# Kernel tuning notes

Measured on AMD Instinct MI355X. Metric: run time of the kernel, lower is better.

## Reference

```python
import jax, jax.numpy as jnp
import numpy as np

NUM_CELLS = 91
NUM_MOVES = 4206
D = 64
NH = 4
HD = D // NH  # 16
FF = 2 * D   # 128
FILTERS = 128

# static hex grid indices (same as torch _hex_grid_indices)
_idx = [(r + 5, q + 5) for q in range(-5, 6) for r in range(-5, 6)
        if max(abs(q), abs(r), abs(q + r)) <= 5]
_HEX_ROWS = np.array([r for r, c in _idx], dtype=np.int32)
_HEX_COLS = np.array([c for r, c in _idx], dtype=np.int32)


def _ln(x, g, b, eps=1e-5):
    m = jnp.mean(x, axis=-1, keepdims=True)
    v = jnp.mean((x - m) ** 2, axis=-1, keepdims=True)
    return (x - m) * jax.lax.rsqrt(v + eps) * g + b


def setup_inputs() -> dict:
    key = jax.random.key(0)
    ks = jax.random.split(key, 24)
    B = 512
    s = lambda fan_in: 1.0 / np.sqrt(fan_in)
    return {
        "x": jax.random.normal(ks[0], (B, FILTERS, 11, 11), dtype=jnp.float32),
        "embed_w": jax.random.uniform(ks[1], (D, FILTERS), minval=-s(FILTERS), maxval=s(FILTERS)),
        "embed_b": jax.random.uniform(ks[2], (D,), minval=-s(FILTERS), maxval=s(FILTERS)),
        "pos": jax.random.normal(ks[3], (1, NUM_CELLS, D)) * 0.02,
        "in_w": jax.random.uniform(ks[4], (3 * D, D), minval=-s(D), maxval=s(D)),
        "in_b": jnp.zeros((3 * D,), jnp.float32),
        "out_w": jax.random.uniform(ks[5], (D, D), minval=-s(D), maxval=s(D)),
        "out_b": jnp.zeros((D,), jnp.float32),
        "ln1_g": jnp.ones((D,), jnp.float32),
        "ln1_b": jnp.zeros((D,), jnp.float32),
        "ln2_g": jnp.ones((D,), jnp.float32),
        "ln2_b": jnp.zeros((D,), jnp.float32),
        "ff1_w": jax.random.uniform(ks[6], (FF, D), minval=-s(D), maxval=s(D)),
        "ff1_b": jax.random.uniform(ks[7], (FF,), minval=-s(D), maxval=s(D)),
        "ff2_w": jax.random.uniform(ks[8], (D, FF), minval=-s(FF), maxval=s(FF)),
        "ff2_b": jax.random.uniform(ks[9], (D,), minval=-s(FF), maxval=s(FF)),
        "from_w": jax.random.uniform(ks[10], (D, D), minval=-s(D), maxval=s(D)),
        "from_b": jax.random.uniform(ks[11], (D,), minval=-s(D), maxval=s(D)),
        "to_w": jax.random.uniform(ks[12], (D, D), minval=-s(D), maxval=s(D)),
        "to_b": jax.random.uniform(ks[13], (D,), minval=-s(D), maxval=s(D)),
        "move_bias": jnp.zeros((NUM_MOVES,), jnp.float32),
        "move_from": jax.random.randint(ks[14], (NUM_MOVES,), 0, NUM_CELLS, dtype=jnp.int32),
        "move_to": jax.random.randint(ks[15], (NUM_MOVES,), 0, NUM_CELLS, dtype=jnp.int32),
    }


def reference(x, embed_w, embed_b, pos, in_w, in_b, out_w, out_b,
              ln1_g, ln1_b, ln2_g, ln2_b, ff1_w, ff1_b, ff2_w, ff2_b,
              from_w, from_b, to_w, to_b, move_bias, move_from, move_to):
    B = x.shape[0]
    # extract_hex: (B, C, 11, 11) -> (B, 91, C)
    feats = x[:, :, _HEX_ROWS, _HEX_COLS].transpose(0, 2, 1)
    h = feats @ embed_w.T + embed_b + pos  # (B, 91, D)

    # TransformerEncoderLayer, norm_first=True, eval (dropout=0), relu FFN
    hn = _ln(h, ln1_g, ln1_b)
    qkv = hn @ in_w.T + in_b  # (B, 91, 3D)
    q, k, v = jnp.split(qkv, 3, axis=-1)
    q = q.reshape(B, NUM_CELLS, NH, HD).transpose(0, 2, 1, 3)
    k = k.reshape(B, NUM_CELLS, NH, HD).transpose(0, 2, 1, 3)
    v = v.reshape(B, NUM_CELLS, NH, HD).transpose(0, 2, 1, 3)
    scores = jnp.einsum("bhqd,bhkd->bhqk", q, k) / np.sqrt(HD)
    attn = jax.nn.softmax(scores, axis=-1)
    o = jnp.einsum("bhqk,bhkd->bhqd", attn, v)
    o = o.transpose(0, 2, 1, 3).reshape(B, NUM_CELLS, D)
    h = h + (o @ out_w.T + out_b)
    hn = _ln(h, ln2_g, ln2_b)
    h = h + (jax.nn.relu(hn @ ff1_w.T + ff1_b) @ ff2_w.T + ff2_b)

    from_feats = h @ from_w.T + from_b  # (B, 91, D)
    to_feats = h @ to_w.T + to_b
    f = jnp.take(from_feats, move_from, axis=1)  # (B, 4206, D)
    t = jnp.take(to_feats, move_to, axis=1)      # (B, 4206, D)
    logits = jnp.sum(f * t, axis=-1) + move_bias  # (B, 4206)
    return logits
```

## Files before the change

### kernel.cpp

```cpp
#include <hip/hip_runtime.h>
#include <hip/hip_bf16.h>

typedef __attribute__((ext_vector_type(8))) short short8;
typedef __attribute__((ext_vector_type(4))) float f32x4;

#define NC    91
#define DM    64
#define CIN   128
#define NMOV  4206
#define MR    96
#define HP    68
#define NT    1024
#define NW    16
#define VTP   104

#define W_EMBED 0
#define W_IN    8192
#define W_OUT   20480
#define W_FF1   24576
#define W_FF2   32768
#define W_FT    40960
#define W_TOTAL 49152

__constant__ int HEXOFF[NC] = {
  55,66,77,88,99,110,
  45,56,67,78,89,100,111,
  35,46,57,68,79,90,101,112,
  25,36,47,58,69,80,91,102,113,
  15,26,37,48,59,70,81,92,103,114,
  5,16,27,38,49,60,71,82,93,104,115,
  6,17,28,39,50,61,72,83,94,105,
  7,18,29,40,51,62,73,84,95,
  8,19,30,41,52,63,74,85,
  9,20,31,42,53,64,75,
  10,21,32,43,54,65
};

#define SWZ(row, col, PB) ((row)*(PB) + ((((((col)*2)>>4)) ^ ((row)&7)) << 4) + (((col)*2)&15))

__device__ __forceinline__ short f2bf(float f) {
  __hip_bfloat16 h = __float2bfloat16(f);
  return __builtin_bit_cast(short, h);
}

__device__ __forceinline__ short8 ldfrag128(const short* buf, int row, int k0) {
  return *(const short8*)((const char*)buf + SWZ(row, k0, 128));
}
__device__ __forceinline__ short8 ldfrag256(const short* buf, int row, int k0) {
  return *(const short8*)((const char*)buf + SWZ(row, k0, 256));
}
__device__ __forceinline__ void stb16_128(short* buf, int row, int col, float v) {
  *(short*)((char*)buf + SWZ(row, col, 128)) = f2bf(v);
}
__device__ __forceinline__ void cp8_swz(short* dst, int PB, const short* src, int r, int c8, int K) {
  short8 v = *(const short8*)(src + r*K + c8*8);
  *(short8*)((char*)dst + r*PB + ((c8 ^ (r&7)) << 4)) = v;
}

__device__ __forceinline__ void ln_group(const float* hbuf, short* ab16,
                                         const float* gw, const float* gb,
                                         int wid, int lane) {
  const int sub = lane >> 4;
  const int l16 = lane & 15;
  const float4 g4 = *(const float4*)&gw[l16*4];
  const float4 b4 = *(const float4*)&gb[l16*4];
  for (int g = wid; g < 23; g += NW) {
    int i = g*4 + sub;
    if (i < NC) {
      float4 v = *(const float4*)&hbuf[i*HP + l16*4];
      float s  = (v.x + v.y) + (v.z + v.w);
      float sq = fmaf(v.x,v.x, fmaf(v.y,v.y, fmaf(v.z,v.z, v.w*v.w)));
      #pragma unroll
      for (int off = 1; off < 16; off <<= 1) {
        s  += __shfl_xor(s, off, 64);
        sq += __shfl_xor(sq, off, 64);
      }
      float m  = s * (1.0f/64.0f);
      float vr = sq * (1.0f/64.0f) - m*m;
      float rs = rsqrtf(vr + 1e-5f);
      short4 o;
      o.x = f2bf((v.x - m)*rs*g4.x + b4.x);
      o.y = f2bf((v.y - m)*rs*g4.y + b4.y);
      o.z = f2bf((v.z - m)*rs*g4.z + b4.z);
      o.w = f2bf((v.w - m)*rs*g4.w + b4.w);
      *(short4*)((char*)ab16 + i*128 + (((l16>>1) ^ (i&7))<<4) + (l16&1)*8) = o;
    }
  }
}

__global__ __launch_bounds__(256)
void prep_w(const float* __restrict__ embed_w, const float* __restrict__ in_w,
            const float* __restrict__ out_w, const float* __restrict__ ff1_w,
            const float* __restrict__ ff2_w, const float* __restrict__ from_w,
            const float* __restrict__ to_w, short* __restrict__ ws)
{
  int i = blockIdx.x*256 + threadIdx.x;
  if (i >= W_TOTAL) return;
  float v;
  if      (i < 8192)  v = embed_w[i];
  else if (i < 20480) v = in_w[i - 8192];
  else if (i < 24576) v = out_w[i - 20480];
  else if (i < 32768) v = ff1_w[i - 24576];
  else if (i < 40960) v = ff2_w[i - 32768];
  else if (i < 45056) v = from_w[i - 40960];
  else                v = to_w[i - 45056];
  ws[i] = f2bf(v);
}

__global__ __launch_bounds__(1024, 1)
void policy_fused(
    const float* __restrict__ x,
    const float* __restrict__ embed_b, const float* __restrict__ pos,
    const float* __restrict__ in_b,  const float* __restrict__ out_b,
    const float* __restrict__ ln1_g, const float* __restrict__ ln1_b,
    const float* __restrict__ ln2_g, const float* __restrict__ ln2_b,
    const float* __restrict__ ff1_b, const float* __restrict__ ff2_b,
    const float* __restrict__ from_b, const float* __restrict__ to_b,
    const float* __restrict__ move_bias,
    const int* __restrict__ move_from, const int* __restrict__ move_to,
    const short* __restrict__ ws,
    float* __restrict__ out)
{
  __shared__ float arena[18816];
  __shared__ float hbuf[MR*HP];
  __shared__ short ab16[MR*64];
  __shared__ short wAll[20480];
  __shared__ float lsum[384];

  const int tid  = threadIdx.x;
  const int lane = tid & 63;
  const int wid  = tid >> 6;
  const int l15  = lane & 15;
  const int kfr  = (lane >> 4) * 8;
  const int mfr  = (lane >> 4) * 4;
  const int b    = blockIdx.x;
  const float* xb = x + (size_t)b * (CIN*121);

  short* arena_s = (short*)arena;
  short* featsb = arena_s;
  short* qf     = arena_s + 24576;
  short* kf     = arena_s + 30720;
  short* vtb    = wAll;
  short* owst   = arena_s + 24576;
  short* f1     = arena_s + 18432;
  float* G      = arena;

  #define PALL_ROW(i) ((char*)((i) < 64 ? (void*)((char*)arena + (i)*768) \
                                        : (void*)((char*)wAll + 16384 + ((i)-64)*768)))

  for (int e = tid; e < 16*NC; e += NT) {
    int c0 = e / NC, i = e - c0*NC;
    float v[8];
    #pragma unroll
    for (int u = 0; u < 8; ++u) v[u] = xb[(c0*8 + u)*121 + HEXOFF[i]];
    short8 s8;
    #pragma unroll
    for (int u = 0; u < 8; ++u) s8[u] = f2bf(v[u]);
    *(short8*)((char*)featsb + i*256 + ((c0 ^ (i&7)) << 4)) = s8;
  }
  if (tid < 320) ((unsigned*)featsb)[5824 + tid] = 0;
  if (tid < 384) lsum[tid] = 0.f;
  for (int e = tid; e < 1024; e += NT) {
    int r = e >> 4, c8 = e & 15;
    cp8_swz(wAll, 256, ws + W_EMBED, r, c8, 128);
  }
  for (int e = tid; e < 1536; e += NT) {
    int r = e >> 3, c8 = e & 7;
    cp8_swz(wAll + 8192, 128, ws + W_IN, r, c8, 64);
  }
  __syncthreads();

  for (int t = wid; t < 24; t += NW) {
    int mt = t >> 2, nt = t & 3;
    int ar = mt*16 + l15, br = nt*16 + l15;
    f32x4 acc = {0.f,0.f,0.f,0.f};
    #pragma unroll
    for (int kk = 0; kk < 4; ++kk) {
      short8 a = ldfrag256(featsb, ar, kk*32 + kfr);
      short8 w = ldfrag256(wAll,   br, kk*32 + kfr);
      acc = __builtin_amdgcn_mfma_f32_16x16x32_bf16(a, w, acc, 0, 0, 0);
    }
    int col = nt*16 + l15;
    float eb = embed_b[col];
    #pragma unroll
    for (int i2 = 0; i2 < 4; ++i2) {
      int m = mt*16 + mfr + i2;
      float p = (m < NC) ? pos[m*DM + col] : 0.f;
      hbuf[m*HP + col] = acc[i2] + eb + p;
    }
  }
  __syncthreads();

  if (tid < 160) ((unsigned*)ab16)[2912 + tid] = 0;
  ln_group(hbuf, ab16, ln1_g, ln1_b, wid, lane);
  __syncthreads();

  {
    const float CS = 0.25f * 1.4426950408889634f;
    for (int t = wid; t < 72; t += NW) {
      int mt = t / 12, nt = t - mt*12;
      int ar = mt*16 + l15, br = nt*16 + l15;
      f32x4 acc = {0.f,0.f,0.f,0.f};
      #pragma unroll
      for (int kk = 0; kk < 2; ++kk) {
        short8 a = ldfrag128(ab16,        ar, kk*32 + kfr);
        short8 w = ldfrag128(wAll + 8192, br, kk*32 + kfr);
        acc = __builtin_amdgcn_mfma_f32_16x16x32_bf16(a, w, acc, 0, 0, 0);
      }
      int col = nt*16 + l15;
      float bia = in_b[col];
      int h = (col & 63) >> 4;
      int d = col & 15;
      if (nt < 4) {
        int base = (h*6 + mt)*32 + ((d >= 8) ? 16 : 0);
        #pragma unroll
        for (int i2 = 0; i2 < 4; ++i2)
          qf[(base + mfr + i2)*8 + (d & 7)] = f2bf((acc[i2] + bia) * CS);
      } else if (nt < 8) {
        int base = (h*6 + mt)*32 + ((d >= 8) ? 16 : 0);
        #pragma unroll
        for (int i2 = 0; i2 < 4; ++i2)
          kf[(base + mfr + i2)*8 + (d & 7)] = f2bf(acc[i2] + bia);
      } else {
        #pragma unroll
        for (int i2 = 0; i2 < 4; ++i2) {
          int m = mt*16 + mfr + i2;
          if (m < NC) vtb[(h*16 + d)*VTP + m] = f2bf(acc[i2] + bia);
        }
      }
    }
    for (int e = tid; e < 832; e += NT) {
      int r = e / 13, c = e - r*13;
      vtb[r*VTP + NC + c] = 0;
    }
  }
  __syncthreads();

  {
    const short8 zfrag = {0,0,0,0,0,0,0,0};
    for (int t = wid; t < 144; t += NW) {
      int h = t / 36, r = t - h*36;
      int it = r / 6, jt = r - it*6;
      short8 a = zfrag, w = zfrag;
      if (lane < 32) {
        a = *(const short8*)(kf + ((h*6 + jt)*32 + lane)*8);
        w = *(const short8*)(qf + ((h*6 + it)*32 + lane)*8);
      }
      f32x4 acc = {0.f,0.f,0.f,0.f};
      acc = __builtin_amdgcn_mfma_f32_16x16x32_bf16(a, w, acc, 0, 0, 0);
      int i  = it*16 + l15;
      int jb = jt*16 + mfr;
      float p0 = exp2f(acc[0]), p1 = exp2f(acc[1]);
      float p2 = exp2f(acc[2]), p3 = exp2f(acc[3]);
      float psum = ((jb+0) < NC ? p0 : 0.f) + ((jb+1) < NC ? p1 : 0.f)
                 + ((jb+2) < NC ? p2 : 0.f) + ((jb+3) < NC ? p3 : 0.f);
      psum += __shfl_xor(psum, 16, 64);
      psum += __shfl_xor(psum, 32, 64);
      if (lane < 16) atomicAdd(&lsum[h*96 + i], psum);
      short4 p4;
      p4.x = f2bf(p0); p4.y = f2bf(p1); p4.z = f2bf(p2); p4.w = f2bf(p3);
      *(short4*)(PALL_ROW(i) + ((((h*96 + jb)*2)) ^ ((i&7) << 4))) = p4;
    }
  }
  __syncthreads();

  for (int e = tid; e < 512; e += NT) {
    int r = e >> 3, c8 = e & 7;
    cp8_swz(owst, 128, ws + W_OUT, r, c8, 64);
  }
  for (int t = wid; t < 24; t += NW) {
    int h = t & 3, it = t >> 2;
    int i = it*16 + l15;
    const char* prow = PALL_ROW(i);
    f32x4 acc = {0.f,0.f,0.f,0.f};
    #pragma unroll
    for (int kk = 0; kk < 3; ++kk) {
      int k0 = kk*32 + kfr;
      short8 a = *(const short8*)(vtb + (h*16 + l15)*VTP + k0);
      short8 w = *(const short8*)(prow + (((h*96 + k0)*2) ^ ((i&7) << 4)));
      acc = __builtin_amdgcn_mfma_f32_16x16x32_bf16(a, w, acc, 0, 0, 0);
    }
    float li = 1.0f / lsum[h*96 + i];
    short4 o4;
    o4.x = f2bf(acc[0] * li); o4.y = f2bf(acc[1] * li);
    o4.z = f2bf(acc[2] * li); o4.w = f2bf(acc[3] * li);
    *(short4*)((char*)ab16 + SWZ(i, h*16 + mfr, 128)) = o4;
  }
  __syncthreads();

  for (int e = tid; e < 1024; e += NT) {
    int r = e >> 3, c8 = e & 7;
    cp8_swz(wAll, 128, ws + W_FF1, r, c8, 64);
  }
  for (int t = wid; t < 24; t += NW) {
    int mt = t >> 2, nt = t & 3;
    int ar = mt*16 + l15, br = nt*16 + l15;
    f32x4 acc = {0.f,0.f,0.f,0.f};
    #pragma unroll
    for (int kk = 0; kk < 2; ++kk) {
      short8 a = ldfrag128(ab16, ar, kk*32 + kfr);
      short8 w = ldfrag128(owst, br, kk*32 + kfr);
      acc = __builtin_amdgcn_mfma_f32_16x16x32_bf16(a, w, acc, 0, 0, 0);
    }
    int col = nt*16 + l15;
    float ob = out_b[col];
    #pragma unroll
    for (int i2 = 0; i2 < 4; ++i2) {
      int m = mt*16 + mfr + i2;
      hbuf[m*HP + col] += acc[i2] + ob;
    }
  }
  __syncthreads();

  ln_group(hbuf, ab16, ln2_g, ln2_b, wid, lane);
  __syncthreads();

  for (int e = tid; e < 1024; e += NT) {
    int r = e >> 4, c8 = e & 15;
    cp8_swz(wAll + 8192, 256, ws + W_FF2, r, c8, 128);
  }
  for (int t = wid; t < 48; t += NW) {
    int mt = t >> 3, nt = t & 7;
    int ar = mt*16 + l15, br = nt*16 + l15;
    f32x4 acc = {0.f,0.f,0.f,0.f};
    #pragma unroll
    for (int kk = 0; kk < 2; ++kk) {
      short8 a = ldfrag128(ab16, ar, kk*32 + kfr);
      short8 w = ldfrag128(wAll, br, kk*32 + kfr);
      acc = __builtin_amdgcn_mfma_f32_16x16x32_bf16(a, w, acc, 0, 0, 0);
    }
    int col = nt*16 + l15;
    float bia = ff1_b[col];
    #pragma unroll
    for (int i2 = 0; i2 < 4; ++i2) {
      int m = mt*16 + mfr + i2;
      *(short*)((char*)f1 + SWZ(m, col, 256)) = f2bf(fmaxf(acc[i2] + bia, 0.f));
    }
  }
  __syncthreads();

  for (int e = tid; e < 1024; e += NT) {
    int r = e >> 3, c8 = e & 7;
    cp8_swz(wAll, 128, ws + W_FT, r, c8, 64);
  }
  for (int t = wid; t < 24; t += NW) {
    int mt = t >> 2, nt = t & 3;
    int ar = mt*16 + l15, br = nt*16 + l15;
    f32x4 acc = {0.f,0.f,0.f,0.f};
    #pragma unroll
    for (int kk = 0; kk < 4; ++kk) {
      short8 a = ldfrag256(f1,          ar, kk*32 + kfr);
      short8 w = ldfrag256(wAll + 8192, br, kk*32 + kfr);
      acc = __builtin_amdgcn_mfma_f32_16x16x32_bf16(a, w, acc, 0, 0, 0);
    }
    int col = nt*16 + l15;
    float bia = ff2_b[col];
    #pragma unroll
    for (int i2 = 0; i2 < 4; ++i2) {
      int m = mt*16 + mfr + i2;
      stb16_128(ab16, m, col, hbuf[m*HP + col] + acc[i2] + bia);
    }
  }
  __syncthreads();

  short* Fb = (short*)hbuf;
  short* Tb = (short*)hbuf + 6144;
  for (int t = wid; t < 48; t += NW) {
    int mt = t >> 3, nt = t & 7;
    int ar = mt*16 + l15, br = nt*16 + l15;
    f32x4 acc = {0.f,0.f,0.f,0.f};
    #pragma unroll
    for (int kk = 0; kk < 2; ++kk) {
      short8 a = ldfrag128(ab16, ar, kk*32 + kfr);
      short8 w = ldfrag128(wAll, br, kk*32 + kfr);
      acc = __builtin_amdgcn_mfma_f32_16x16x32_bf16(a, w, acc, 0, 0, 0);
    }
    int col = nt*16 + l15;
    if (nt < 4) {
      float bia = from_b[col];
      #pragma unroll
      for (int i2 = 0; i2 < 4; ++i2)
        stb16_128(Fb, mt*16 + mfr + i2, col, acc[i2] + bia);
    } else {
      int c2 = col - 64;
      float bia = to_b[c2];
      #pragma unroll
      for (int i2 = 0; i2 < 4; ++i2)
        stb16_128(Tb, mt*16 + mfr + i2, c2, acc[i2] + bia);
    }
  }
  __syncthreads();

  for (int t = wid; t < 36; t += NW) {
    int mt = t / 6, nt = t - mt*6;
    int ar = mt*16 + l15, br = nt*16 + l15;
    f32x4 acc = {0.f,0.f,0.f,0.f};
    #pragma unroll
    for (int kk = 0; kk < 2; ++kk) {
      short8 a = ldfrag128(Fb, ar, kk*32 + kfr);
      short8 w = ldfrag128(Tb, br, kk*32 + kfr);
      acc = __builtin_amdgcn_mfma_f32_16x16x32_bf16(a, w, acc, 0, 0, 0);
    }
    int col = nt*16 + l15;
    #pragma unroll
    for (int i2 = 0; i2 < 4; ++i2)
      G[(mt*16 + mfr + i2)*96 + col] = acc[i2];
  }
  __syncthreads();

  {
    float* ob = out + (size_t)b * NMOV;
    for (int m = tid; m < NMOV; m += NT) {
      ob[m] = G[move_from[m]*96 + move_to[m]] + move_bias[m];
    }
  }
  #undef PALL_ROW
}

extern "C" void kernel_launch(void* const* d_in, const int* in_sizes, int n_in,
                              void* d_out, int out_size, void* d_ws, size_t ws_size,
                              hipStream_t stream) {
  const float* x        = (const float*)d_in[0];
  const float* embed_w  = (const float*)d_in[1];
  const float* embed_b  = (const float*)d_in[2];
  const float* pos      = (const float*)d_in[3];
  const float* in_w     = (const float*)d_in[4];
  const float* in_b     = (const float*)d_in[5];
  const float* out_w    = (const float*)d_in[6];
  const float* out_b    = (const float*)d_in[7];
  const float* ln1_g    = (const float*)d_in[8];
  const float* ln1_b    = (const float*)d_in[9];
  const float* ln2_g    = (const float*)d_in[10];
  const float* ln2_b    = (const float*)d_in[11];
  const float* ff1_w    = (const float*)d_in[12];
  const float* ff1_b    = (const float*)d_in[13];
  const float* ff2_w    = (const float*)d_in[14];
  const float* ff2_b    = (const float*)d_in[15];
  const float* from_w   = (const float*)d_in[16];
  const float* from_b   = (const float*)d_in[17];
  const float* to_w     = (const float*)d_in[18];
  const float* to_b     = (const float*)d_in[19];
  const float* move_bias= (const float*)d_in[20];
  const int*   move_from= (const int*)d_in[21];
  const int*   move_to  = (const int*)d_in[22];

  short* wsb = (short*)d_ws;
  prep_w<<<dim3((W_TOTAL + 255)/256), dim3(256), 0, stream>>>(
      embed_w, in_w, out_w, ff1_w, ff2_w, from_w, to_w, wsb);

  int B = in_sizes[0] / (CIN * 121);
  policy_fused<<<dim3(B), dim3(NT), 0, stream>>>(
      x, embed_b, pos, in_b, out_b,
      ln1_g, ln1_b, ln2_g, ln2_b, ff1_b, ff2_b,
      from_b, to_b, move_bias, move_from, move_to,
      (const short*)wsb, (float*)d_out);
}
```

Before: 53.85 us.

## Shrink LDS footprint via region reuse, keep residual in registers, per-head attention

Replaces the large fixed shared-memory arrays with one ~72KB arena whose regions are reused across stages. The residual stream now stays in registers, and layer norm statistics come from shuffle-reduced partial sums. Attention is processed one head at a time, with a per-head V transpose and P buffer, to cut LDS use. The aim is to fit two blocks per CU instead of one, at the cost of extra syncthreads, serialised per-head phases, and only 6 waves busy in the PV step.

```diff
diff --git a/kernel.cpp b/kernel.cpp
--- a/kernel.cpp
+++ b/kernel.cpp
@@ -8,11 +8,14 @@
 #define DM    64
 #define CIN   128
 #define NMOV  4206
-#define MR    96
-#define HP    68
 #define NT    1024
 #define NW    16
-#define VTP   104
+
+#define OFF_R2 0
+#define OFF_R1 34944
+#define OFF_PH 56944
+#define OFF_SE 59856
+#define LDS_SZ 72144
 
 #define W_EMBED 0
 #define W_IN    8192
@@ -42,6 +45,9 @@
   __hip_bfloat16 h = __float2bfloat16(f);
   return __builtin_bit_cast(short, h);
 }
+__device__ __forceinline__ float bfs(short v) {
+  return __builtin_bit_cast(float, ((unsigned)(unsigned short)v) << 16);
+}
 
 __device__ __forceinline__ short8 ldfrag128(const short* buf, int row, int k0) {
   return *(const short8*)((const char*)buf + SWZ(row, k0, 128));
@@ -51,41 +57,19 @@
 }
 __device__ __forceinline__ void stb16_128(short* buf, int row, int col, float v) {
   *(short*)((char*)buf + SWZ(row, col, 128)) = f2bf(v);
+}
+__device__ __forceinline__ short8 ld_qkv8(const short* q, int r, int col) {
+  return *(const short8*)((const char*)q + r*384 + ((((col*2)>>4) ^ (r&7)) << 4));
+}
+__device__ __forceinline__ void st_qkv(short* q, int r, int col, short v) {
+  *(short*)((char*)q + r*384 + ((((col*2)>>4) ^ (r&7)) << 4) + ((col*2)&15)) = v;
+}
+__device__ __forceinline__ short ld_qkv1(const short* q, int r, int col) {
+  return *(const short*)((const char*)q + r*384 + ((((col*2)>>4) ^ (r&7)) << 4) + ((col*2)&15));
 }
 __device__ __forceinline__ void cp8_swz(short* dst, int PB, const short* src, int r, int c8, int K) {
   short8 v = *(const short8*)(src + r*K + c8*8);
   *(short8*)((char*)dst + r*PB + ((c8 ^ (r&7)) << 4)) = v;
-}
-
-__device__ __forceinline__ void ln_group(const float* hbuf, short* ab16,
-                                         const float* gw, const float* gb,
-                                         int wid, int lane) {
-  const int sub = lane >> 4;
-  const int l16 = lane & 15;
-  const float4 g4 = *(const float4*)&gw[l16*4];
-  const float4 b4 = *(const float4*)&gb[l16*4];
-  for (int g = wid; g < 23; g += NW) {
-    int i = g*4 + sub;
-    if (i < NC) {
-      float4 v = *(const float4*)&hbuf[i*HP + l16*4];
-      float s  = (v.x + v.y) + (v.z + v.w);
-      float sq = fmaf(v.x,v.x, fmaf(v.y,v.y, fmaf(v.z,v.z, v.w*v.w)));
-      #pragma unroll
-      for (int off = 1; off < 16; off <<= 1) {
-        s  += __shfl_xor(s, off, 64);
-        sq += __shfl_xor(sq, off, 64);
-      }
-      float m  = s * (1.0f/64.0f);
-      float vr = sq * (1.0f/64.0f) - m*m;
-      float rs = rsqrtf(vr + 1e-5f);
-      short4 o;
-      o.x = f2bf((v.x - m)*rs*g4.x + b4.x);
-      o.y = f2bf((v.y - m)*rs*g4.y + b4.y);
-      o.z = f2bf((v.z - m)*rs*g4.z + b4.z);
-      o.w = f2bf((v.w - m)*rs*g4.w + b4.w);
-      *(short4*)((char*)ab16 + i*128 + (((l16>>1) ^ (i&7))<<4) + (l16&1)*8) = o;
-    }
-  }
 }
 
 __global__ __launch_bounds__(256)
@@ -107,7 +91,7 @@
   ws[i] = f2bf(v);
 }
 
-__global__ __launch_bounds__(1024, 1)
+__global__ __launch_bounds__(1024, 8)
 void policy_fused(
     const float* __restrict__ x,
     const float* __restrict__ embed_b, const float* __restrict__ pos,
@@ -121,11 +105,17 @@
     const short* __restrict__ ws,
     float* __restrict__ out)
 {
-  __shared__ float arena[18816];
-  __shared__ float hbuf[MR*HP];
-  __shared__ short ab16[MR*64];
-  __shared__ short wAll[20480];
-  __shared__ float lsum[384];
+  __shared__ __align__(16) char LDSA[LDS_SZ];
+
+  short* R2s = (short*)(LDSA + OFF_R2);
+  short* R1s = (short*)(LDSA + OFF_R1);
+  float* ph  = (float*)(LDSA + OFF_PH);
+  short* ab  = (short*)(LDSA + OFF_SE);
+  short* Pb  = R1s;
+  short* vt  = R1s + 9464;
+  float* G   = (float*)R1s;
+  short* Fb  = R2s;
+  short* Tb  = R2s + 5824;
 
   const int tid  = threadIdx.x;
   const int lane = tid & 63;
@@ -135,18 +125,13 @@
   const int mfr  = (lane >> 4) * 4;
   const int b    = blockIdx.x;
   const float* xb = x + (size_t)b * (CIN*121);
-
-  short* arena_s = (short*)arena;
-  short* featsb = arena_s;
-  short* qf     = arena_s + 24576;
-  short* kf     = arena_s + 30720;
-  short* vtb    = wAll;
-  short* owst   = arena_s + 24576;
-  short* f1     = arena_s + 18432;
-  float* G      = arena;
-
-  #define PALL_ROW(i) ((char*)((i) < 64 ? (void*)((char*)arena + (i)*768) \
-                                        : (void*)((char*)wAll + 16384 + ((i)-64)*768)))
+  const short8 zfrag = {0,0,0,0,0,0,0,0};
+
+  f32x4 hreg0 = {0.f,0.f,0.f,0.f};
+  f32x4 hreg1 = {0.f,0.f,0.f,0.f};
+  const int mt0 = wid >> 2,        nt0 = wid & 3;
+  const int mt1 = (wid + 16) >> 2, nt1 = (wid + 16) & 3;
+  const int col0 = nt0*16 + l15, col1 = nt1*16 + l15;
 
   for (int e = tid; e < 16*NC; e += NT) {
     int c0 = e / NC, i = e - c0*NC;
@@ -156,17 +141,142 @@
     short8 s8;
     #pragma unroll
     for (int u = 0; u < 8; ++u) s8[u] = f2bf(v[u]);
-    *(short8*)((char*)featsb + i*256 + ((c0 ^ (i&7)) << 4)) = s8;
-  }
-  if (tid < 320) ((unsigned*)featsb)[5824 + tid] = 0;
-  if (tid < 384) lsum[tid] = 0.f;
+    *(short8*)((char*)R2s + i*256 + ((c0 ^ (i&7)) << 4)) = s8;
+  }
+  if (tid < 320) ((unsigned*)R2s)[5824 + tid] = 0;
   for (int e = tid; e < 1024; e += NT) {
     int r = e >> 4, c8 = e & 15;
-    cp8_swz(wAll, 256, ws + W_EMBED, r, c8, 128);
-  }
-  for (int e = tid; e < 1536; e += NT) {
+    cp8_swz(R1s, 256, ws + W_EMBED, r, c8, 128);
+  }
+  __syncthreads();
+
+  {
+    {
+      int ar = mt0*16 + l15, br = nt0*16 + l15;
+      f32x4 acc = {0.f,0.f,0.f,0.f};
+      #pragma unroll
+      for (int kk = 0; kk < 4; ++kk) {
+        short8 a = ldfrag256(R2s, ar, kk*32 + kfr);
+        short8 w = ldfrag256(R1s, br, kk*32 + kfr);
+        acc = __builtin_amdgcn_mfma_f32_16x16x32_bf16(a, w, acc, 0, 0, 0);
+      }
+      float eb = embed_b[col0];
+      #pragma unroll
+      for (int i2 = 0; i2 < 4; ++i2) {
+        int m = mt0*16 + mfr + i2;
+        hreg0[i2] = acc[i2] + eb + ((m < NC) ? pos[m*DM + col0] : 0.f);
+      }
+      #pragma unroll
+      for (int i2 = 0; i2 < 4; ++i2) {
+        float s = hreg0[i2], q = s*s;
+        #pragma unroll
+        for (int off = 1; off < 16; off <<= 1) {
+          s += __shfl_xor(s, off, 64);
+          q += __shfl_xor(q, off, 64);
+        }
+        int m = mt0*16 + mfr + i2;
+        if (l15 == 0 && m < NC) { ph[m*8 + nt0*2] = s; ph[m*8 + nt0*2 + 1] = q; }
+      }
+    }
+    if (wid < 8) {
+      int ar = mt1*16 + l15, br = nt1*16 + l15;
+      f32x4 acc = {0.f,0.f,0.f,0.f};
+      #pragma unroll
+      for (int kk = 0; kk < 4; ++kk) {
+        short8 a = ldfrag256(R2s, ar, kk*32 + kfr);
+        short8 w = ldfrag256(R1s, br, kk*32 + kfr);
+        acc = __builtin_amdgcn_mfma_f32_16x16x32_bf16(a, w, acc, 0, 0, 0);
+      }
+      float eb = embed_b[col1];
+      #pragma unroll
+      for (int i2 = 0; i2 < 4; ++i2) {
+        int m = mt1*16 + mfr + i2;
+        hreg1[i2] = acc[i2] + eb + ((m < NC) ? pos[m*DM + col1] : 0.f);
+      }
+      #pragma unroll
+      for (int i2 = 0; i2 < 4; ++i2) {
+        float s = hreg1[i2], q = s*s;
+        #pragma unroll
+        for (int off = 1; off < 16; off <<= 1) {
+          s += __shfl_xor(s, off, 64);
+          q += __shfl_xor(q, off, 64);
+        }
+        int m = mt1*16 + mfr + i2;
+        if (l15 == 0 && m < NC) { ph[m*8 + nt1*2] = s; ph[m*8 + nt1*2 + 1] = q; }
+      }
+    }
+  }
+  __syncthreads();
+
+  for (int e = tid; e < 1024; e += NT) {
     int r = e >> 3, c8 = e & 7;
-    cp8_swz(wAll + 8192, 128, ws + W_IN, r, c8, 64);
+    cp8_swz(R1s, 128, ws + W_IN, r, c8, 64);
+  }
+  {
+    {
+      float g1 = ln1_g[col0], b1 = ln1_b[col0];
+      #pragma unroll
+      for (int i2 = 0; i2 < 4; ++i2) {
+        int m = mt0*16 + mfr + i2;
+        if (m < NC) {
+          float4 pa = *(const float4*)&ph[m*8];
+          float4 pb = *(const float4*)&ph[m*8 + 4];
+          float s = (pa.x + pa.z) + (pb.x + pb.z);
+          float q = (pa.y + pa.w) + (pb.y + pb.w);
+          float mean = s * (1.0f/64.0f);
+          float var  = q * (1.0f/64.0f) - mean*mean;
+          float rs   = rsqrtf(var + 1e-5f);
+          stb16_128(ab, m, col0, (hreg0[i2] - mean)*rs*g1 + b1);
+        }
+      }
+    }
+    if (wid < 8) {
+      float g1 = ln1_g[col1], b1 = ln1_b[col1];
+      #pragma unroll
+      for (int i2 = 0; i2 < 4; ++i2) {
+        int m = mt1*16 + mfr + i2;
+        if (m < NC) {
+          float4 pa = *(const float4*)&ph[m*8];
+          float4 pb = *(const float4*)&ph[m*8 + 4];
+          float s = (pa.x + pa.z) + (pb.x + pb.z);
+          float q = (pa.y + pa.w) + (pb.y + pb.w);
+          float mean = s * (1.0f/64.0f);
+          float var  = q * (1.0f/64.0f) - mean*mean;
+          float rs   = rsqrtf(var + 1e-5f);
+          stb16_128(ab, m, col1, (hreg1[i2] - mean)*rs*g1 + b1);
+        }
+      }
+    }
+  }
+  __syncthreads();
+
+  {
+    const float CS = 0.25f * 1.4426950408889634f;
+    for (int t = wid; t < 48; t += NW) {
+      int mt = t >> 3, nt = t & 7;
+      int ar = mt*16 + l15, br = nt*16 + l15;
+      f32x4 acc = {0.f,0.f,0.f,0.f};
+      #pragma unroll
+      for (int kk = 0; kk < 2; ++kk) {
+        short8 a = ldfrag128(ab,  ar, kk*32 + kfr);
+        short8 w = ldfrag128(R1s, br, kk*32 + kfr);
+        acc = __builtin_amdgcn_mfma_f32_16x16x32_bf16(a, w, acc, 0, 0, 0);
+      }
+      int col = nt*16 + l15;
+      float bia = in_b[col];
+      float sc = (col < 64) ? CS : 1.0f;
+      #pragma unroll
+      for (int i2 = 0; i2 < 4; ++i2) {
+        int m = mt*16 + mfr + i2;
+        if (m < NC) st_qkv(R2s, m, col, f2bf((acc[i2] + bia) * sc));
+      }
+    }
+  }
+  __syncthreads();
+
+  for (int e = tid; e < 512; e += NT) {
+    int r = e >> 3, c8 = e & 7;
+    cp8_swz(R1s, 128, ws + W_IN + 8192, r, c8, 64);
   }
   __syncthreads();
 
@@ -175,158 +285,189 @@
     int ar = mt*16 + l15, br = nt*16 + l15;
     f32x4 acc = {0.f,0.f,0.f,0.f};
     #pragma unroll
-    for (int kk = 0; kk < 4; ++kk) {
-      short8 a = ldfrag256(featsb, ar, kk*32 + kfr);
-      short8 w = ldfrag256(wAll,   br, kk*32 + kfr);
+    for (int kk = 0; kk < 2; ++kk) {
+      short8 a = ldfrag128(ab,  ar, kk*32 + kfr);
+      short8 w = ldfrag128(R1s, br, kk*32 + kfr);
       acc = __builtin_amdgcn_mfma_f32_16x16x32_bf16(a, w, acc, 0, 0, 0);
     }
     int col = nt*16 + l15;
-    float eb = embed_b[col];
+    float bia = in_b[128 + col];
     #pragma unroll
     for (int i2 = 0; i2 < 4; ++i2) {
       int m = mt*16 + mfr + i2;
-      float p = (m < NC) ? pos[m*DM + col] : 0.f;
-      hbuf[m*HP + col] = acc[i2] + eb + p;
-    }
-  }
-  __syncthreads();
-
-  if (tid < 160) ((unsigned*)ab16)[2912 + tid] = 0;
-  ln_group(hbuf, ab16, ln1_g, ln1_b, wid, lane);
-  __syncthreads();
-
-  {
-    const float CS = 0.25f * 1.4426950408889634f;
-    for (int t = wid; t < 72; t += NW) {
-      int mt = t / 12, nt = t - mt*12;
-      int ar = mt*16 + l15, br = nt*16 + l15;
-      f32x4 acc = {0.f,0.f,0.f,0.f};
-      #pragma unroll
-      for (int kk = 0; kk < 2; ++kk) {
-        short8 a = ldfrag128(ab16,        ar, kk*32 + kfr);
-        short8 w = ldfrag128(wAll + 8192, br, kk*32 + kfr);
-        acc = __builtin_amdgcn_mfma_f32_16x16x32_bf16(a, w, acc, 0, 0, 0);
-      }
-      int col = nt*16 + l15;
-      float bia = in_b[col];
-      int h = (col & 63) >> 4;
-      int d = col & 15;
-      if (nt < 4) {
-        int base = (h*6 + mt)*32 + ((d >= 8) ? 16 : 0);
-        #pragma unroll
-        for (int i2 = 0; i2 < 4; ++i2)
-          qf[(base + mfr + i2)*8 + (d & 7)] = f2bf((acc[i2] + bia) * CS);
-      } else if (nt < 8) {
-        int base = (h*6 + mt)*32 + ((d >= 8) ? 16 : 0);
-        #pragma unroll
-        for (int i2 = 0; i2 < 4; ++i2)
-          kf[(base + mfr + i2)*8 + (d & 7)] = f2bf(acc[i2] + bia);
-      } else {
-        #pragma unroll
-        for (int i2 = 0; i2 < 4; ++i2) {
-          int m = mt*16 + mfr + i2;
-          if (m < NC) vtb[(h*16 + d)*VTP + m] = f2bf(acc[i2] + bia);
-        }
-      }
-    }
-    for (int e = tid; e < 832; e += NT) {
-      int r = e / 13, c = e - r*13;
-      vtb[r*VTP + NC + c] = 0;
-    }
-  }
-  __syncthreads();
-
-  {
-    const short8 zfrag = {0,0,0,0,0,0,0,0};
-    for (int t = wid; t < 144; t += NW) {
-      int h = t / 36, r = t - h*36;
-      int it = r / 6, jt = r - it*6;
+      if (m < NC) st_qkv(R2s, m, 128 + col, f2bf(acc[i2] + bia));
+    }
+  }
+  __syncthreads();
+
+  for (int h = 0; h < 4; ++h) {
+    if (h == 0) {
+      for (int e = tid; e < 455; e += NT) {
+        int i = e / 5, c = 91 + (e - (e/5)*5);
+        Pb[i*104 + c] = 0;
+      }
+    }
+    for (int e = tid; e < 1536; e += NT) {
+      int d = e / 96, j = e - d*96;
+      vt[d*96 + j] = (j < NC) ? ld_qkv1(R2s, j, 128 + h*16 + d) : (short)0;
+    }
+    for (int t = wid; t < 36; t += NW) {
+      int it = t / 6, jt = t - it*6;
       short8 a = zfrag, w = zfrag;
       if (lane < 32) {
-        a = *(const short8*)(kf + ((h*6 + jt)*32 + lane)*8);
-        w = *(const short8*)(qf + ((h*6 + it)*32 + lane)*8);
+        a = ld_qkv8(R2s, jt*16 + l15, 64 + h*16 + ((lane >> 4) << 3));
+        w = ld_qkv8(R2s, it*16 + l15, h*16 + ((lane >> 4) << 3));
       }
       f32x4 acc = {0.f,0.f,0.f,0.f};
       acc = __builtin_amdgcn_mfma_f32_16x16x32_bf16(a, w, acc, 0, 0, 0);
-      int i  = it*16 + l15;
-      int jb = jt*16 + mfr;
+      int i = it*16 + l15;
       float p0 = exp2f(acc[0]), p1 = exp2f(acc[1]);
       float p2 = exp2f(acc[2]), p3 = exp2f(acc[3]);
+      int jb = jt*16 + mfr;
       float psum = ((jb+0) < NC ? p0 : 0.f) + ((jb+1) < NC ? p1 : 0.f)
                  + ((jb+2) < NC ? p2 : 0.f) + ((jb+3) < NC ? p3 : 0.f);
       psum += __shfl_xor(psum, 16, 64);
       psum += __shfl_xor(psum, 32, 64);
-      if (lane < 16) atomicAdd(&lsum[h*96 + i], psum);
-      short4 p4;
-      p4.x = f2bf(p0); p4.y = f2bf(p1); p4.z = f2bf(p2); p4.w = f2bf(p3);
-      *(short4*)(PALL_ROW(i) + ((((h*96 + jb)*2)) ^ ((i&7) << 4))) = p4;
-    }
-  }
-  __syncthreads();
+      if (i < NC) {
+        if ((jb+0) < NC) Pb[i*104 + jb+0] = f2bf(p0);
+        if ((jb+1) < NC) Pb[i*104 + jb+1] = f2bf(p1);
+        if ((jb+2) < NC) Pb[i*104 + jb+2] = f2bf(p2);
+        if ((jb+3) < NC) Pb[i*104 + jb+3] = f2bf(p3);
+        if (lane < 16) ph[i*8 + jt] = psum;
+      }
+    }
+    __syncthreads();
+
+    for (int t = wid; t < 6; t += NW) {
+      f32x4 acc = {0.f,0.f,0.f,0.f};
+      #pragma unroll
+      for (int kk = 0; kk < 3; ++kk) {
+        int k0 = kk*32 + kfr;
+        short8 a = *(const short8*)(vt + l15*96 + k0);
+        short8 w = *(const short8*)((const char*)Pb + (t*16 + l15)*208 + k0*2);
+        acc = __builtin_amdgcn_mfma_f32_16x16x32_bf16(a, w, acc, 0, 0, 0);
+      }
+      int i = t*16 + l15;
+      if (i < NC) {
+        float ls = ((ph[i*8+0] + ph[i*8+1]) + (ph[i*8+2] + ph[i*8+3]))
+                 + (ph[i*8+4] + ph[i*8+5]);
+        float li = 1.0f / ls;
+        #pragma unroll
+        for (int i2 = 0; i2 < 4; ++i2)
+          stb16_128(ab, i, h*16 + mfr + i2, acc[i2] * li);
+      }
+    }
+    __syncthreads();
+  }
 
   for (int e = tid; e < 512; e += NT) {
     int r = e >> 3, c8 = e & 7;
-    cp8_swz(owst, 128, ws + W_OUT, r, c8, 64);
-  }
-  for (int t = wid; t < 24; t += NW) {
-    int h = t & 3, it = t >> 2;
-    int i = it*16 + l15;
-    const char* prow = PALL_ROW(i);
-    f32x4 acc = {0.f,0.f,0.f,0.f};
-    #pragma unroll
-    for (int kk = 0; kk < 3; ++kk) {
-      int k0 = kk*32 + kfr;
-      short8 a = *(const short8*)(vtb + (h*16 + l15)*VTP + k0);
-      short8 w = *(const short8*)(prow + (((h*96 + k0)*2) ^ ((i&7) << 4)));
-      acc = __builtin_amdgcn_mfma_f32_16x16x32_bf16(a, w, acc, 0, 0, 0);
-    }
-    float li = 1.0f / lsum[h*96 + i];
-    short4 o4;
-    o4.x = f2bf(acc[0] * li); o4.y = f2bf(acc[1] * li);
-    o4.z = f2bf(acc[2] * li); o4.w = f2bf(acc[3] * li);
-    *(short4*)((char*)ab16 + SWZ(i, h*16 + mfr, 128)) = o4;
+    cp8_swz(R1s, 128, ws + W_OUT, r, c8, 64);
+  }
+  __syncthreads();
+
+  {
+    {
+      int ar = mt0*16 + l15, br = nt0*16 + l15;
+      f32x4 acc = {0.f,0.f,0.f,0.f};
+      #pragma unroll
+      for (int kk = 0; kk < 2; ++kk) {
+        short8 a = ldfrag128(ab,  ar, kk*32 + kfr);
+        short8 w = ldfrag128(R1s, br, kk*32 + kfr);
+        acc = __builtin_amdgcn_mfma_f32_16x16x32_bf16(a, w, acc, 0, 0, 0);
+      }
+      float ob = out_b[col0];
+      #pragma unroll
+      for (int i2 = 0; i2 < 4; ++i2) hreg0[i2] += acc[i2] + ob;
+      #pragma unroll
+      for (int i2 = 0; i2 < 4; ++i2) {
+        float s = hreg0[i2], q = s*s;
+        #pragma unroll
+        for (int off = 1; off < 16; off <<= 1) {
+          s += __shfl_xor(s, off, 64);
+          q += __shfl_xor(q, off, 64);
+        }
+        int m = mt0*16 + mfr + i2;
+        if (l15 == 0 && m < NC) { ph[m*8 + nt0*2] = s; ph[m*8 + nt0*2 + 1] = q; }
+      }
+    }
+    if (wid < 8) {
+      int ar = mt1*16 + l15, br = nt1*16 + l15;
+      f32x4 acc = {0.f,0.f,0.f,0.f};
+      #pragma unroll
+      for (int kk = 0; kk < 2; ++kk) {
+        short8 a = ldfrag128(ab,  ar, kk*32 + kfr);
+        short8 w = ldfrag128(R1s, br, kk*32 + kfr);
+        acc = __builtin_amdgcn_mfma_f32_16x16x32_bf16(a, w, acc, 0, 0, 0);
+      }
+      float ob = out_b[col1];
+      #pragma unroll
+      for (int i2 = 0; i2 < 4; ++i2) hreg1[i2] += acc[i2] + ob;
+      #pragma unroll
+      for (int i2 = 0; i2 < 4; ++i2) {
+        float s = hreg1[i2], q = s*s;
+        #pragma unroll
+        for (int off = 1; off < 16; off <<= 1) {
+          s += __shfl_xor(s, off, 64);
+          q += __shfl_xor(q, off, 64);
+        }
+        int m = mt1*16 + mfr + i2;
+        if (l15 == 0 && m < NC) { ph[m*8 + nt1*2] = s; ph[m*8 + nt1*2 + 1] = q; }
+      }
+    }
   }
   __syncthreads();
 
   for (int e = tid; e < 1024; e += NT) {
     int r = e >> 3, c8 = e & 7;
-    cp8_swz(wAll, 128, ws + W_FF1, r, c8, 64);
-  }
-  for (int t = wid; t < 24; t += NW) {
-    int mt = t >> 2, nt = t & 3;
-    int ar = mt*16 + l15, br = nt*16 + l15;
-    f32x4 acc = {0.f,0.f,0.f,0.f};
-    #pragma unroll
-    for (int kk = 0; kk < 2; ++kk) {
-      short8 a = ldfrag128(ab16, ar, kk*32 + kfr);
-      short8 w = ldfrag128(owst, br, kk*32 + kfr);
-      acc = __builtin_amdgcn_mfma_f32_16x16x32_bf16(a, w, acc, 0, 0, 0);
-    }
-    int col = nt*16 + l15;
-    float ob = out_b[col];
-    #pragma unroll
-    for (int i2 = 0; i2 < 4; ++i2) {
-      int m = mt*16 + mfr + i2;
-      hbuf[m*HP + col] += acc[i2] + ob;
-    }
-  }
-  __syncthreads();
-
-  ln_group(hbuf, ab16, ln2_g, ln2_b, wid, lane);
-  __syncthreads();
-
-  for (int e = tid; e < 1024; e += NT) {
-    int r = e >> 4, c8 = e & 15;
-    cp8_swz(wAll + 8192, 256, ws + W_FF2, r, c8, 128);
-  }
+    cp8_swz(R1s, 128, ws + W_FF1, r, c8, 64);
+  }
+  {
+    {
+      float g2 = ln2_g[col0], b2 = ln2_b[col0];
+      #pragma unroll
+      for (int i2 = 0; i2 < 4; ++i2) {
+        int m = mt0*16 + mfr + i2;
+        if (m < NC) {
+          float4 pa = *(const float4*)&ph[m*8];
+          float4 pb = *(const float4*)&ph[m*8 + 4];
+          float s = (pa.x + pa.z) + (pb.x + pb.z);
+          float q = (pa.y + pa.w) + (pb.y + pb.w);
+          float mean = s * (1.0f/64.0f);
+          float var  = q * (1.0f/64.0f) - mean*mean;
+          float rs   = rsqrtf(var + 1e-5f);
+          stb16_128(ab, m, col0, (hreg0[i2] - mean)*rs*g2 + b2);
+        }
+      }
+    }
+    if (wid < 8) {
+      float g2 = ln2_g[col1], b2 = ln2_b[col1];
+      #pragma unroll
+      for (int i2 = 0; i2 < 4; ++i2) {
+        int m = mt1*16 + mfr + i2;
+        if (m < NC) {
+          float4 pa = *(const float4*)&ph[m*8];
+          float4 pb = *(const float4*)&ph[m*8 + 4];
+          float s = (pa.x + pa.z) + (pb.x + pb.z);
+          float q = (pa.y + pa.w) + (pb.y + pb.w);
+          float mean = s * (1.0f/64.0f);
+          float var  = q * (1.0f/64.0f) - mean*mean;
+          float rs   = rsqrtf(var + 1e-5f);
+          stb16_128(ab, m, col1, (hreg1[i2] - mean)*rs*g2 + b2);
+        }
+      }
+    }
+  }
+  __syncthreads();
+
   for (int t = wid; t < 48; t += NW) {
     int mt = t >> 3, nt = t & 7;
     int ar = mt*16 + l15, br = nt*16 + l15;
     f32x4 acc = {0.f,0.f,0.f,0.f};
     #pragma unroll
     for (int kk = 0; kk < 2; ++kk) {
-      short8 a = ldfrag128(ab16, ar, kk*32 + kfr);
-      short8 w = ldfrag128(wAll, br, kk*32 + kfr);
+      short8 a = ldfrag128(ab,  ar, kk*32 + kfr);
+      short8 w = ldfrag128(R1s, br, kk*32 + kfr);
       acc = __builtin_amdgcn_mfma_f32_16x16x32_bf16(a, w, acc, 0, 0, 0);
     }
     int col = nt*16 + l15;
@@ -334,59 +475,86 @@
     #pragma unroll
     for (int i2 = 0; i2 < 4; ++i2) {
       int m = mt*16 + mfr + i2;
-      *(short*)((char*)f1 + SWZ(m, col, 256)) = f2bf(fmaxf(acc[i2] + bia, 0.f));
+      if (m < NC)
+        *(short*)((char*)R2s + SWZ(m, col, 256)) = f2bf(fmaxf(acc[i2] + bia, 0.f));
+    }
+  }
+  __syncthreads();
+
+  for (int e = tid; e < 1024; e += NT) {
+    int r = e >> 4, c8 = e & 15;
+    cp8_swz(R1s, 256, ws + W_FF2, r, c8, 128);
+  }
+  __syncthreads();
+
+  {
+    {
+      int ar = mt0*16 + l15, br = nt0*16 + l15;
+      f32x4 acc = {0.f,0.f,0.f,0.f};
+      #pragma unroll
+      for (int kk = 0; kk < 4; ++kk) {
+        short8 a = ldfrag256(R2s, ar, kk*32 + kfr);
+        short8 w = ldfrag256(R1s, br, kk*32 + kfr);
+        acc = __builtin_amdgcn_mfma_f32_16x16x32_bf16(a, w, acc, 0, 0, 0);
+      }
+      float bia = ff2_b[col0];
+      #pragma unroll
+      for (int i2 = 0; i2 < 4; ++i2) {
+        int m = mt0*16 + mfr + i2;
+        if (m < NC) stb16_128(ab, m, col0, hreg0[i2] + acc[i2] + bia);
+      }
+    }
+    if (wid < 8) {
+      int ar = mt1*16 + l15, br = nt1*16 + l15;
+      f32x4 acc = {0.f,0.f,0.f,0.f};
+      #pragma unroll
+      for (int kk = 0; kk < 4; ++kk) {
+        short8 a = ldfrag256(R2s, ar, kk*32 + kfr);
+        short8 w = ldfrag256(R1s, br, kk*32 + kfr);
+        acc = __builtin_amdgcn_mfma_f32_16x16x32_bf16(a, w, acc, 0, 0, 0);
+      }
+      float bia = ff2_b[col1];
+      #pragma unroll
+      for (int i2 = 0; i2 < 4; ++i2) {
+        int m = mt1*16 + mfr + i2;
+        if (m < NC) stb16_128(ab, m, col1, hreg1[i2] + acc[i2] + bia);
+      }
     }
   }
   __syncthreads();
 
   for (int e = tid; e < 1024; e += NT) {
     int r = e >> 3, c8 = e & 7;
-    cp8_swz(wAll, 128, ws + W_FT, r, c8, 64);
-  }
-  for (int t = wid; t < 24; t += NW) {
-    int mt = t >> 2, nt = t & 3;
-    int ar = mt*16 + l15, br = nt*16 + l15;
-    f32x4 acc = {0.f,0.f,0.f,0.f};
-    #pragma unroll
-    for (int kk = 0; kk < 4; ++kk) {
-      short8 a = ldfrag256(f1,          ar, kk*32 + kfr);
-      short8 w = ldfrag256(wAll + 8192, br, kk*32 + kfr);
-      acc = __builtin_amdgcn_mfma_f32_16x16x32_bf16(a, w, acc, 0, 0, 0);
-    }
-    int col = nt*16 + l15;
-    float bia = ff2_b[col];
-    #pragma unroll
-    for (int i2 = 0; i2 < 4; ++i2) {
-      int m = mt*16 + mfr + i2;
-      stb16_128(ab16, m, col, hbuf[m*HP + col] + acc[i2] + bia);
-    }
-  }
-  __syncthreads();
-
-  short* Fb = (short*)hbuf;
-  short* Tb = (short*)hbuf + 6144;
+    cp8_swz(R1s, 128, ws + W_FT, r, c8, 64);
+  }
+  __syncthreads();
+
   for (int t = wid; t < 48; t += NW) {
     int mt = t >> 3, nt = t & 7;
     int ar = mt*16 + l15, br = nt*16 + l15;
     f32x4 acc = {0.f,0.f,0.f,0.f};
     #pragma unroll
     for (int kk = 0; kk < 2; ++kk) {
-      short8 a = ldfrag128(ab16, ar, kk*32 + kfr);
-      short8 w = ldfrag128(wAll, br, kk*32 + kfr);
+      short8 a = ldfrag128(ab,  ar, kk*32 + kfr);
+      short8 w = ldfrag128(R1s, br, kk*32 + kfr);
       acc = __builtin_amdgcn_mfma_f32_16x16x32_bf16(a, w, acc, 0, 0, 0);
     }
     int col = nt*16 + l15;
     if (nt < 4) {
       float bia = from_b[col];
       #pragma unroll
-      for (int i2 = 0; i2 < 4; ++i2)
-        stb16_128(Fb, mt*16 + mfr + i2, col, acc[i2] + bia);
+      for (int i2 = 0; i2 < 4; ++i2) {
+        int m = mt*16 + mfr + i2;
+        if (m < NC) stb16_128(Fb, m, col, acc[i2] + bia);
+      }
     } else {
       int c2 = col - 64;
       float bia = to_b[c2];
       #pragma unroll
-      for (int i2 = 0; i2 < 4; ++i2)
-        stb16_128(Tb, mt*16 + mfr + i2, c2, acc[i2] + bia);
+      for (int i2 = 0; i2 < 4; ++i2) {
+        int m = mt*16 + mfr + i2;
+        if (m < NC) stb16_128(Tb, m, c2, acc[i2] + bia);
+      }
     }
   }
   __syncthreads();
@@ -403,8 +571,10 @@
     }
     int col = nt*16 + l15;
     #pragma unroll
-    for (int i2 = 0; i2 < 4; ++i2)
-      G[(mt*16 + mfr + i2)*96 + col] = acc[i2];
+    for (int i2 = 0; i2 < 4; ++i2) {
+      int m = mt*16 + mfr + i2;
+      if (m < NC) G[m*96 + col] = acc[i2];
+    }
   }
   __syncthreads();
 
@@ -414,7 +584,6 @@
       ob[m] = G[move_from[m]*96 + move_to[m]] + move_bias[m];
     }
   }
-  #undef PALL_ROW
 }
 
 extern "C" void kernel_launch(void* const* d_in, const int* in_sizes, int n_in,
```

Result: slower. 63.11 us (+17.2%).
